# Kernel tuning notes

Measured on AMD Instinct MI355X. Metric: run time of the kernel, lower is better.

## Reference

```python
import jax, jax.numpy as jnp
import numpy as np

N = 100000
IN_C = 128
HID_C = 128
OUT_C = 128
E = 3200000


def setup_inputs() -> dict:
    key = jax.random.key(0)
    ks = jax.random.split(key, 8)
    x = jax.random.normal(ks[0], (N, IN_C), dtype=jnp.float32)
    edge_index = jax.random.randint(ks[1], (2, E), 0, N, dtype=jnp.int64)
    edge_weight = jnp.ones((E,), dtype=jnp.float32)
    s = 1.0 / np.sqrt(HID_C)
    W_conv = jax.random.uniform(ks[2], (HID_C, IN_C), jnp.float32, -s, s)
    b_conv = jnp.zeros((HID_C,), dtype=jnp.float32)
    W_fc = jax.random.uniform(ks[3], (HID_C, HID_C), jnp.float32, -s, s)
    b_fc = jax.random.uniform(ks[4], (HID_C,), jnp.float32, -s, s)
    W_fc2 = jax.random.uniform(ks[5], (OUT_C, HID_C), jnp.float32, -s, s)
    b_fc2 = jax.random.uniform(ks[6], (OUT_C,), jnp.float32, -s, s)
    return {"x": x, "edge_index": edge_index, "edge_weight": edge_weight,
            "W_conv": W_conv, "b_conv": b_conv, "W_fc": W_fc, "b_fc": b_fc,
            "W_fc2": W_fc2, "b_fc2": b_fc2}


def _gcn_conv(x, edge_index, edge_weight, W_conv, b_conv):
    n = x.shape[0]
    # add self-loops with weight 1 (PyG GCNConv default)
    loop = jnp.arange(n, dtype=edge_index.dtype)
    src = jnp.concatenate([edge_index[0], loop])
    dst = jnp.concatenate([edge_index[1], loop])
    ew = jnp.concatenate([edge_weight, jnp.ones((n,), dtype=edge_weight.dtype)])
    # symmetric normalization: deg^-1/2[src] * w * deg^-1/2[dst]
    deg = jax.ops.segment_sum(ew, dst, num_segments=n)
    dinv = jnp.where(deg > 0, jax.lax.rsqrt(jnp.where(deg > 0, deg, 1.0)), 0.0)
    norm = dinv[src] * ew * dinv[dst]  # [E+N]
    h = x @ W_conv.T                   # [N, hid], bias-free linear first
    msg = h[src] * norm[:, None]       # gather + scale
    agg = jax.ops.segment_sum(msg, dst, num_segments=n)  # scatter-add
    return agg + b_conv


def reference(x, edge_index, edge_weight, W_conv, b_conv, W_fc, b_fc, W_fc2, b_fc2):
    h = _gcn_conv(x, edge_index, edge_weight, W_conv, b_conv)
    h = jax.nn.relu(h)
    h = jax.nn.relu(h @ W_fc.T + b_fc)
    return h @ W_fc2.T + b_fc2
```

## Files before the change

kernel.cpp:

```cpp
#include <hip/hip_runtime.h>

typedef short bf16x8 __attribute__((ext_vector_type(8)));
typedef short bf16x4 __attribute__((ext_vector_type(4)));
typedef float f32x4 __attribute__((ext_vector_type(4)));
typedef float f32x2 __attribute__((ext_vector_type(2)));

#define PS 32
#define CAPP 1312
#define NB 256
#define CAPB 17536

__device__ __forceinline__ unsigned short f2bf(float f) {
    unsigned int u = __float_as_uint(f);
    u = (u + 0x7FFFu + ((u >> 16) & 1u)) >> 16;
    return (unsigned short)u;
}

__global__ __launch_bounds__(1024) void scatA_k(const int* __restrict__ ei,
                                                const float* __restrict__ ew,
                                                int* __restrict__ bucketCnt,
                                                int2* __restrict__ bstage,
                                                const float* __restrict__ Wc,
                                                const float* __restrict__ Wf,
                                                const float* __restrict__ W2,
                                                unsigned short* __restrict__ wcb,
                                                unsigned short* __restrict__ wfb,
                                                unsigned short* __restrict__ w2b,
                                                int E, int NBK, int EPB) {
    __shared__ int cntl[256];
    __shared__ int basel[256];
    const int b = blockIdx.x, tid = threadIdx.x;

    if (b < 12) {
        int t = (b << 10) | tid;
        int a = t >> 12, idx = t & 4095;
        const float4* s4 = (const float4*)(a == 0 ? Wc : (a == 1 ? Wf : W2));
        unsigned short* dw = (a == 0 ? wcb : (a == 1 ? wfb : w2b));
        float4 v = s4[idx];
        ushort4 o;
        o.x = f2bf(v.x); o.y = f2bf(v.y); o.z = f2bf(v.z); o.w = f2bf(v.w);
        *(ushort4*)(dw + idx * 4) = o;
    }

    if (tid < 256) cntl[tid] = 0;
    __syncthreads();
    const int s = b * EPB, e = min(E, s + EPB);
    for (int i = s + tid; i < e; i += 1024)
        atomicAdd(&cntl[ei[E + i] >> 9], 1);
    __syncthreads();
    if (tid < NBK) {
        int c = cntl[tid];
        basel[tid] = tid * CAPB + (c ? atomicAdd(&bucketCnt[tid], c) : 0);
        cntl[tid] = 0;
    }
    __syncthreads();
    for (int i = s + tid; i < e; i += 1024) {
        int src = ei[i];
        int dst = ei[E + i];
        float w = ew[i];
        int bk = dst >> 9;
        int lidx = atomicAdd(&cntl[bk], 1);
        int pos = basel[bk] + lidx;
        if (pos < (bk + 1) * CAPB)
            bstage[pos] = make_int2(src | ((dst & 511) << 17), __float_as_int(w));
    }
}

__global__ __launch_bounds__(1024) void scatB_k(const int* __restrict__ bucketCnt,
                                                const int2* __restrict__ bstage,
                                                int* __restrict__ partCnt,
                                                int* __restrict__ nodeOff,
                                                float* __restrict__ dinv,
                                                int2* __restrict__ regions,
                                                int P, int N) {
    __shared__ int cnode[512];
    __shared__ float degf[512];
    const int bk = blockIdx.x, tid = threadIdx.x;
    const int cnt = min(bucketCnt[bk], CAPB);
    const int2* bs = bstage + (size_t)bk * CAPB;

    if (tid < 512) { cnode[tid] = 0; degf[tid] = 0.f; }
    __syncthreads();
    for (int i = tid; i < cnt; i += 1024) {
        int2 r = bs[i];
        int nl = ((unsigned)r.x >> 17) & 511;
        atomicAdd(&cnode[nl], 1);
        atomicAdd(&degf[nl], __int_as_float(r.y));
    }
    __syncthreads();
    if (tid < 512) {
        int cn = cnode[tid];
        int v = cn;
#pragma unroll
        for (int off = 1; off < 32; off <<= 1) {
            int u = __shfl_up(v, off, 32);
            if ((tid & 31) >= off) v += u;
        }
        int n = bk * 512 + tid;
        if (n < N) {
            nodeOff[n] = v - cn;
            dinv[n] = rsqrtf(1.0f + degf[tid]);
        }
        if ((tid & 31) == 31) {
            int p = bk * 16 + (tid >> 5);
            if (p < P) partCnt[p] = v;
        }
        cnode[tid] = v - cn;
    }
    __syncthreads();
    for (int i = tid; i < cnt; i += 1024) {
        int2 r = bs[i];
        unsigned x = (unsigned)r.x;
        int nl = (x >> 17) & 511;
        int pos = atomicAdd(&cnode[nl], 1);
        if (pos < CAPP) {
            int p = bk * 16 + (nl >> 5);
            regions[(size_t)p * CAPP + pos] = make_int2((int)((x & 0x1FFFFu) << 7), r.y);
        }
    }
}

__global__ __launch_bounds__(256) void dgemm1_k(const float* __restrict__ x,
                                                const unsigned short* __restrict__ Wcb,
                                                const float* __restrict__ dinv,
                                                unsigned short* __restrict__ h,
                                                int M) {
    __shared__ __align__(16) unsigned short Wl[128 * 136];
    __shared__ float dl64[64];
    const int tid = threadIdx.x;

    if (tid < 64) {
        int node = blockIdx.x * 64 + tid;
        dl64[tid] = (node < M) ? dinv[node] : 0.f;
    }

#pragma unroll
    for (int i = 0; i < 8; ++i) {
        int c = i * 256 + tid;
        int r = c >> 4, col = (c & 15) * 8;
        *(bf16x8*)&Wl[r * 136 + col] = *(const bf16x8*)(Wcb + c * 8);
    }
    __syncthreads();

    const int wave = tid >> 6, lane = tid & 63;
    const int m = lane & 15, quad = lane >> 4;
    const int rowBase = blockIdx.x * 64 + wave * 16;
    int arow = rowBase + m;
    int arowc = arow < M ? arow : (M - 1);

    bf16x8 afrag[4];
    const float* pa = x + (size_t)arowc * 128 + quad * 8;
#pragma unroll
    for (int kc = 0; kc < 4; ++kc) {
        float4 v0 = *(const float4*)(pa + kc * 32);
        float4 v1 = *(const float4*)(pa + kc * 32 + 4);
        bf16x8 f;
        f[0] = (short)f2bf(v0.x); f[1] = (short)f2bf(v0.y);
        f[2] = (short)f2bf(v0.z); f[3] = (short)f2bf(v0.w);
        f[4] = (short)f2bf(v1.x); f[5] = (short)f2bf(v1.y);
        f[6] = (short)f2bf(v1.z); f[7] = (short)f2bf(v1.w);
        afrag[kc] = f;
    }

    float dv[4];
#pragma unroll
    for (int r = 0; r < 4; ++r)
        dv[r] = dl64[wave * 16 + quad * 4 + r];

#pragma unroll
    for (int nt = 0; nt < 8; ++nt) {
        f32x4 acc = {0.f, 0.f, 0.f, 0.f};
        const unsigned short* wb = &Wl[(nt * 16 + m) * 136 + quad * 8];
#pragma unroll
        for (int kc = 0; kc < 4; ++kc) {
            bf16x8 bfrag = *(const bf16x8*)(wb + kc * 32);
            acc = __builtin_amdgcn_mfma_f32_16x16x32_bf16(afrag[kc], bfrag, acc, 0, 0, 0);
        }
        const int col = nt * 16 + m;
#pragma unroll
        for (int r = 0; r < 4; ++r) {
            int row = rowBase + quad * 4 + r;
            if (row < M)
                h[((size_t)(col >> 6) * M + row) * 64 + (col & 63)] = f2bf(acc[r] * dv[r]);
        }
    }
}

__global__ __launch_bounds__(256) void aggF_k(const int* __restrict__ partCnt,
                                              const int* __restrict__ nodeOff,
                                              const int2* __restrict__ regions,
                                              const unsigned short* __restrict__ h,
                                              const float* __restrict__ dinv,
                                              const float* __restrict__ bconv,
                                              unsigned short* __restrict__ h2, int N) {
    __shared__ __align__(16) int2 stag[CAPP];
    __shared__ int cstart[PS + 1];
    const int p = blockIdx.x, tid = threadIdx.x;
    const int cnt = min(partCnt[p], CAPP);
    const int2* reg = regions + (size_t)p * CAPP;

    if (tid < PS) {
        int node = p * PS + tid;
        cstart[tid] = (node < N) ? nodeOff[node] : cnt;
    } else if (tid == PS) {
        cstart[PS] = cnt;
    }
    for (int i = tid; i < cnt; i += 256) stag[i] = reg[i];
    __syncthreads();

    const int wave = tid >> 6, lane = tid & 63;
    const int g = lane >> 4;
    const int c4 = (lane & 15) * 4;
    const int c4b = c4 * 2;

#define ACC2(q, w) {                                                        \
        unsigned ux = (unsigned)(q).x, uy = (unsigned)(q).y;                \
        f32x2 ww; ww[0] = (w); ww[1] = (w);                                 \
        f32x2 v01, v23;                                                     \
        v01[0] = __uint_as_float(ux << 16);                                 \
        v01[1] = __uint_as_float(ux & 0xFFFF0000u);                         \
        v23[0] = __uint_as_float(uy << 16);                                 \
        v23[1] = __uint_as_float(uy & 0xFFFF0000u);                         \
        a01 = v01 * ww + a01; a23 = v23 * ww + a23; }

#pragma unroll
    for (int hh = 0; hh < 2; ++hh) {
        const char* hb = (const char*)h + ((size_t)hh * (size_t)N << 7);
        for (int nl = wave; nl < PS; nl += 4) {
            int n = p * PS + nl;
            if (n >= N) continue;
            const int s = cstart[nl], e = cstart[nl + 1];
            f32x2 a01 = {0.f, 0.f}, a23 = {0.f, 0.f};
            int j = s;
            const int e32 = s + ((e - s) & ~31);
            for (; j < e32; j += 32) {
                int2 r0 = stag[j + g];
                int2 r1 = stag[j + 4 + g];
                int2 r2 = stag[j + 8 + g];
                int2 r3 = stag[j + 12 + g];
                int2 r4 = stag[j + 16 + g];
                int2 r5 = stag[j + 20 + g];
                int2 r6 = stag[j + 24 + g];
                int2 r7 = stag[j + 28 + g];
                int2 q0 = *(const int2*)(hb + ((unsigned)r0.x + c4b));
                int2 q1 = *(const int2*)(hb + ((unsigned)r1.x + c4b));
                int2 q2 = *(const int2*)(hb + ((unsigned)r2.x + c4b));
                int2 q3 = *(const int2*)(hb + ((unsigned)r3.x + c4b));
                int2 q4 = *(const int2*)(hb + ((unsigned)r4.x + c4b));
                int2 q5 = *(const int2*)(hb + ((unsigned)r5.x + c4b));
                int2 q6 = *(const int2*)(hb + ((unsigned)r6.x + c4b));
                int2 q7 = *(const int2*)(hb + ((unsigned)r7.x + c4b));
                ACC2(q0, __int_as_float(r0.y));
                ACC2(q1, __int_as_float(r1.y));
                ACC2(q2, __int_as_float(r2.y));
                ACC2(q3, __int_as_float(r3.y));
                ACC2(q4, __int_as_float(r4.y));
                ACC2(q5, __int_as_float(r5.y));
                ACC2(q6, __int_as_float(r6.y));
                ACC2(q7, __int_as_float(r7.y));
            }
            const int e16 = s + ((e - s) & ~15);
            for (; j < e16; j += 16) {
                int2 r0 = stag[j + g];
                int2 r1 = stag[j + 4 + g];
                int2 r2 = stag[j + 8 + g];
                int2 r3 = stag[j + 12 + g];
                int2 q0 = *(const int2*)(hb + ((unsigned)r0.x + c4b));
                int2 q1 = *(const int2*)(hb + ((unsigned)r1.x + c4b));
                int2 q2 = *(const int2*)(hb + ((unsigned)r2.x + c4b));
                int2 q3 = *(const int2*)(hb + ((unsigned)r3.x + c4b));
                ACC2(q0, __int_as_float(r0.y));
                ACC2(q1, __int_as_float(r1.y));
                ACC2(q2, __int_as_float(r2.y));
                ACC2(q3, __int_as_float(r3.y));
            }
            for (; j < e; j += 8) {
                int j0 = j + g, j1 = j + 4 + g;
                int2 r0 = stag[j0 < e ? j0 : s];
                int2 r1 = stag[j1 < e ? j1 : s];
                float w0 = (j0 < e) ? __int_as_float(r0.y) : 0.f;
                float w1 = (j1 < e) ? __int_as_float(r1.y) : 0.f;
                int2 q0 = *(const int2*)(hb + ((unsigned)r0.x + c4b));
                int2 q1 = *(const int2*)(hb + ((unsigned)r1.x + c4b));
                ACC2(q0, w0);
                ACC2(q1, w1);
            }
            float acc[4] = {a01[0], a01[1], a23[0], a23[1]};
#pragma unroll
            for (int k = 0; k < 4; ++k) {
                float v = acc[k];
                v += __shfl_xor(v, 16, 64);
                v += __shfl_xor(v, 32, 64);
                acc[k] = v;
            }
            if (g == 0) {
                float di = dinv[n];
                int2 qs = *(const int2*)(hb + (((size_t)(unsigned)n << 7) + c4b));
                float4 b = *(const float4*)(bconv + hh * 64 + c4);
                unsigned ux = (unsigned)qs.x, uy = (unsigned)qs.y;
                bf16x4 o;
                o[0] = (short)f2bf(fmaxf(di * (acc[0] + __uint_as_float(ux << 16)) + b.x, 0.f));
                o[1] = (short)f2bf(fmaxf(di * (acc[1] + __uint_as_float(ux & 0xFFFF0000u)) + b.y, 0.f));
                o[2] = (short)f2bf(fmaxf(di * (acc[2] + __uint_as_float(uy << 16)) + b.z, 0.f));
                o[3] = (short)f2bf(fmaxf(di * (acc[3] + __uint_as_float(uy & 0xFFFF0000u)) + b.w, 0.f));
                *(bf16x4*)(h2 + (size_t)n * 128 + hh * 64 + c4) = o;
            }
        }
    }
#undef ACC2
}

__global__ __launch_bounds__(256) void gemm23_k(const unsigned short* __restrict__ h2,
                                                const unsigned short* __restrict__ Wfb,
                                                const float* __restrict__ bfc,
                                                const unsigned short* __restrict__ W2b,
                                                const float* __restrict__ b2,
                                                float* __restrict__ out, int M) {
    __shared__ __align__(16) unsigned short Wl[128 * 136];
    __shared__ __align__(16) unsigned short Tl[64 * 136];
    const int tid = threadIdx.x;

#pragma unroll
    for (int i = 0; i < 8; ++i) {
        int c = i * 256 + tid;
        int r = c >> 4, col = (c & 15) * 8;
        *(bf16x8*)&Wl[r * 136 + col] = *(const bf16x8*)(Wfb + c * 8);
    }
    __syncthreads();

    const int wave = tid >> 6, lane = tid & 63;
    const int m = lane & 15, quad = lane >> 4;
    const int rowBase = blockIdx.x * 64 + wave * 16;
    int arow = rowBase + m;
    int arowc = arow < M ? arow : (M - 1);

    bf16x8 afrag[4];
    {
        const unsigned short* pa = h2 + (size_t)arowc * 128 + quad * 8;
#pragma unroll
        for (int kc = 0; kc < 4; ++kc)
            afrag[kc] = *(const bf16x8*)(pa + kc * 32);
    }

#pragma unroll
    for (int nt = 0; nt < 8; ++nt) {
        f32x4 acc = {0.f, 0.f, 0.f, 0.f};
        const unsigned short* wb = &Wl[(nt * 16 + m) * 136 + quad * 8];
#pragma unroll
        for (int kc = 0; kc < 4; ++kc) {
            bf16x8 bfrag = *(const bf16x8*)(wb + kc * 32);
            acc = __builtin_amdgcn_mfma_f32_16x16x32_bf16(afrag[kc], bfrag, acc, 0, 0, 0);
        }
        const int col = nt * 16 + m;
        float bv = bfc[col];
#pragma unroll
        for (int r = 0; r < 4; ++r) {
            int rowl = wave * 16 + quad * 4 + r;
            Tl[rowl * 136 + col] = f2bf(fmaxf(acc[r] + bv, 0.f));
        }
    }
    __syncthreads();

#pragma unroll
    for (int i = 0; i < 8; ++i) {
        int c = i * 256 + tid;
        int r = c >> 4, col = (c & 15) * 8;
        *(bf16x8*)&Wl[r * 136 + col] = *(const bf16x8*)(W2b + c * 8);
    }
    __syncthreads();

    bf16x8 afrag2[4];
    {
        const unsigned short* pa = &Tl[(wave * 16 + m) * 136 + quad * 8];
#pragma unroll
        for (int kc = 0; kc < 4; ++kc)
            afrag2[kc] = *(const bf16x8*)(pa + kc * 32);
    }
#pragma unroll
    for (int nt = 0; nt < 8; ++nt) {
        f32x4 acc = {0.f, 0.f, 0.f, 0.f};
        const unsigned short* wb = &Wl[(nt * 16 + m) * 136 + quad * 8];
#pragma unroll
        for (int kc = 0; kc < 4; ++kc) {
            bf16x8 bfrag = *(const bf16x8*)(wb + kc * 32);
            acc = __builtin_amdgcn_mfma_f32_16x16x32_bf16(afrag2[kc], bfrag, acc, 0, 0, 0);
        }
        const int col = nt * 16 + m;
        float bv = b2[col];
#pragma unroll
        for (int r = 0; r < 4; ++r) {
            int row = rowBase + quad * 4 + r;
            if (row < M)
                out[(size_t)row * 128 + col] = acc[r] + bv;
        }
    }
}

extern "C" void kernel_launch(void* const* d_in, const int* in_sizes, int n_in,
                              void* d_out, int out_size, void* d_ws, size_t ws_size,
                              hipStream_t stream) {
    const float* x  = (const float*)d_in[0];
    const int* ei   = (const int*)d_in[1];
    const float* ew = (const float*)d_in[2];
    const float* Wc = (const float*)d_in[3];
    const float* bc = (const float*)d_in[4];
    const float* Wf = (const float*)d_in[5];
    const float* bf = (const float*)d_in[6];
    const float* W2 = (const float*)d_in[7];
    const float* b2 = (const float*)d_in[8];
    float* out = (float*)d_out;

    const int N = in_sizes[0] / 128;
    const int E = in_sizes[2];
    const int P = (N + PS - 1) / PS;
    const int NBK = (N + 511) >> 9;

    auto align256 = [](size_t v) { return (v + 255) & ~(size_t)255; };
    char* ws = (char*)d_ws;
    size_t off = 0;
    float* dinv  = (float*)(ws + off); off += align256((size_t)N * 4);
    int* nodeOff = (int*)(ws + off);   off += align256((size_t)N * 4);
    int* partCnt = (int*)(ws + off);   off += align256((size_t)P * 4);
    int* bucketCnt = (int*)(ws + off); off += align256((size_t)NBK * 4);
    unsigned short* wcb = (unsigned short*)(ws + off); off += align256(16384 * 2);
    unsigned short* wfb = (unsigned short*)(ws + off); off += align256(16384 * 2);
    unsigned short* w2b = (unsigned short*)(ws + off); off += align256(16384 * 2);
    unsigned short* h  = (unsigned short*)(ws + off); off += (size_t)N * 256;
    unsigned short* h2 = (unsigned short*)(ws + off);

    int2* bstage = (int2*)h;

    int2* regions = (int2*)out;

    const int EPB = (E + NB - 1) / NB;

    hipMemsetAsync(bucketCnt, 0, (size_t)NBK * 4, stream);
    scatA_k<<<NB, 1024, 0, stream>>>(ei, ew, bucketCnt, bstage, Wc, Wf, W2, wcb, wfb, w2b, E, NBK, EPB);
    scatB_k<<<NBK, 1024, 0, stream>>>(bucketCnt, bstage, partCnt, nodeOff, dinv, regions, P, N);
    dgemm1_k<<<(N + 63) / 64, 256, 0, stream>>>(x, wcb, dinv, h, N);
    aggF_k<<<P, 256, 0, stream>>>(partCnt, nodeOff, regions, h, dinv, bc, h2, N);
    gemm23_k<<<(N + 63) / 64, 256, 0, stream>>>(h2, wfb, bf, w2b, b2, out, N);
}
```

Before: 353.1 us.

## Fuse first GEMM into scatter kernel and defer per-node sorting to aggregation

The first GEMM (x·Wc) is merged into the edge-bucketing kernel as extra blocks, so it runs concurrently with the scatter instead of as a separate launch after it. Because h no longer depends on dinv, the source-side normalization moves into aggF, which applies dinv[src] to each edge weight while staging, and the self-loop term is scaled by di². scatB now writes only per-partition cursors with the local node id packed into each entry, and aggF does the per-node ordering through shared-memory atomics. bstage is relocated to the h2 region so it no longer aliases h. The cost is an extra dinv gather per edge in aggF and a larger fused kernel whose blocks contend for resources.

```diff
diff --git a/kernel.cpp b/kernel.cpp
--- a/kernel.cpp
+++ b/kernel.cpp
@@ -16,53 +16,107 @@
     return (unsigned short)u;
 }
 
-__global__ __launch_bounds__(1024) void scatA_k(const int* __restrict__ ei,
-                                                const float* __restrict__ ew,
-                                                int* __restrict__ bucketCnt,
-                                                int2* __restrict__ bstage,
-                                                const float* __restrict__ Wc,
-                                                const float* __restrict__ Wf,
-                                                const float* __restrict__ W2,
-                                                unsigned short* __restrict__ wcb,
-                                                unsigned short* __restrict__ wfb,
-                                                unsigned short* __restrict__ w2b,
-                                                int E, int NBK, int EPB) {
-    __shared__ int cntl[256];
-    __shared__ int basel[256];
+__global__ __launch_bounds__(1024) void mega_k(const int* __restrict__ ei,
+                                               const float* __restrict__ ew,
+                                               int* __restrict__ bucketCnt,
+                                               int2* __restrict__ bstage,
+                                               const float* __restrict__ x,
+                                               const float* __restrict__ Wc,
+                                               const float* __restrict__ Wf,
+                                               const float* __restrict__ W2,
+                                               unsigned short* __restrict__ wfb,
+                                               unsigned short* __restrict__ w2b,
+                                               unsigned short* __restrict__ h,
+                                               int E, int M, int NBK, int EPB) {
+    __shared__ __align__(16) unsigned short Wl[128 * 136];
     const int b = blockIdx.x, tid = threadIdx.x;
 
-    if (b < 12) {
-        int t = (b << 10) | tid;
-        int a = t >> 12, idx = t & 4095;
-        const float4* s4 = (const float4*)(a == 0 ? Wc : (a == 1 ? Wf : W2));
-        unsigned short* dw = (a == 0 ? wcb : (a == 1 ? wfb : w2b));
-        float4 v = s4[idx];
-        ushort4 o;
-        o.x = f2bf(v.x); o.y = f2bf(v.y); o.z = f2bf(v.z); o.w = f2bf(v.w);
-        *(ushort4*)(dw + idx * 4) = o;
-    }
-
-    if (tid < 256) cntl[tid] = 0;
-    __syncthreads();
-    const int s = b * EPB, e = min(E, s + EPB);
-    for (int i = s + tid; i < e; i += 1024)
-        atomicAdd(&cntl[ei[E + i] >> 9], 1);
-    __syncthreads();
-    if (tid < NBK) {
-        int c = cntl[tid];
-        basel[tid] = tid * CAPB + (c ? atomicAdd(&bucketCnt[tid], c) : 0);
-        cntl[tid] = 0;
-    }
-    __syncthreads();
-    for (int i = s + tid; i < e; i += 1024) {
-        int src = ei[i];
-        int dst = ei[E + i];
-        float w = ew[i];
-        int bk = dst >> 9;
-        int lidx = atomicAdd(&cntl[bk], 1);
-        int pos = basel[bk] + lidx;
-        if (pos < (bk + 1) * CAPB)
-            bstage[pos] = make_int2(src | ((dst & 511) << 17), __float_as_int(w));
+    if (b < NB) {
+        int* cntl = (int*)Wl;
+        int* basel = cntl + 256;
+        if (b < 8) {
+            int t = (b << 10) | tid;
+            int a = t >> 12, idx = t & 4095;
+            const float4* s4 = (const float4*)(a == 0 ? Wf : W2);
+            unsigned short* dw = (a == 0 ? wfb : w2b);
+            float4 v = s4[idx];
+            ushort4 o;
+            o.x = f2bf(v.x); o.y = f2bf(v.y); o.z = f2bf(v.z); o.w = f2bf(v.w);
+            *(ushort4*)(dw + idx * 4) = o;
+        }
+        if (tid < 256) cntl[tid] = 0;
+        __syncthreads();
+        const int s = b * EPB, e = min(E, s + EPB);
+        for (int i = s + tid; i < e; i += 1024)
+            atomicAdd(&cntl[ei[E + i] >> 9], 1);
+        __syncthreads();
+        if (tid < NBK) {
+            int c = cntl[tid];
+            basel[tid] = tid * CAPB + (c ? atomicAdd(&bucketCnt[tid], c) : 0);
+            cntl[tid] = 0;
+        }
+        __syncthreads();
+        for (int i = s + tid; i < e; i += 1024) {
+            int src = ei[i];
+            int dst = ei[E + i];
+            float w = ew[i];
+            int bk = dst >> 9;
+            int lidx = atomicAdd(&cntl[bk], 1);
+            int pos = basel[bk] + lidx;
+            if (pos < (bk + 1) * CAPB)
+                bstage[pos] = make_int2(src | ((dst & 511) << 17), __float_as_int(w));
+        }
+    } else {
+        const int gb = b - NB;
+#pragma unroll
+        for (int i = 0; i < 4; ++i) {
+            int e4 = i * 1024 + tid;
+            float4 v = ((const float4*)Wc)[e4];
+            int el = e4 * 4, r = el >> 7, cc = el & 127;
+            unsigned short* pp = &Wl[r * 136 + cc];
+            pp[0] = f2bf(v.x); pp[1] = f2bf(v.y); pp[2] = f2bf(v.z); pp[3] = f2bf(v.w);
+        }
+        __syncthreads();
+
+        const int wave = tid >> 6, lane = tid & 63;
+        const int m = lane & 15, quad = lane >> 4;
+        const int rowBase = gb * 256 + wave * 16;
+        if (rowBase < M) {
+            int arow = rowBase + m;
+            int arowc = arow < M ? arow : (M - 1);
+
+            bf16x8 afrag[4];
+            const float* pa = x + (size_t)arowc * 128 + quad * 8;
+#pragma unroll
+            for (int kc = 0; kc < 4; ++kc) {
+                float4 v0 = *(const float4*)(pa + kc * 32);
+                float4 v1 = *(const float4*)(pa + kc * 32 + 4);
+                bf16x8 f;
+                f[0] = (short)f2bf(v0.x); f[1] = (short)f2bf(v0.y);
+                f[2] = (short)f2bf(v0.z); f[3] = (short)f2bf(v0.w);
+                f[4] = (short)f2bf(v1.x); f[5] = (short)f2bf(v1.y);
+                f[6] = (short)f2bf(v1.z); f[7] = (short)f2bf(v1.w);
+                afrag[kc] = f;
+            }
+
+#pragma unroll
+            for (int nt = 0; nt < 8; ++nt) {
+                f32x4 acc = {0.f, 0.f, 0.f, 0.f};
+                const unsigned short* wb = &Wl[(nt * 16 + m) * 136 + quad * 8];
+#pragma unroll
+                for (int kc = 0; kc < 4; ++kc) {
+                    bf16x8 bfrag = *(const bf16x8*)(wb + kc * 32);
+                    acc = __builtin_amdgcn_mfma_f32_16x16x32_bf16(afrag[kc], bfrag, acc, 0, 0, 0);
+                }
+                const int col = nt * 16 + m;
+#pragma unroll
+                for (int r = 0; r < 4; ++r) {
+                    int row = rowBase + quad * 4 + r;
+                    if (row < M)
+                        h[((size_t)(col >> 6) * M + row) * 64 + (col & 63)] = f2bf(acc[r]);
+                }
+            }
+        }
     }
 }
 
@@ -75,11 +129,13 @@
                                                 int P, int N) {
     __shared__ int cnode[512];
     __shared__ float degf[512];
+    __shared__ int cur[16];
     const int bk = blockIdx.x, tid = threadIdx.x;
     const int cnt = min(bucketCnt[bk], CAPB);
     const int2* bs = bstage + (size_t)bk * CAPB;
 
     if (tid < 512) { cnode[tid] = 0; degf[tid] = 0.f; }
+    if (tid < 16) cur[tid] = 0;
     __syncthreads();
     for (int i = tid; i < cnt; i += 1024) {
         int2 r = bs[i];
@@ -105,83 +161,18 @@
             int p = bk * 16 + (tid >> 5);
             if (p < P) partCnt[p] = v;
         }
-        cnode[tid] = v - cn;
     }
     __syncthreads();
     for (int i = tid; i < cnt; i += 1024) {
         int2 r = bs[i];
-        unsigned x = (unsigned)r.x;
-        int nl = (x >> 17) & 511;
-        int pos = atomicAdd(&cnode[nl], 1);
+        unsigned xx = (unsigned)r.x;
+        int nl = (xx >> 17) & 511;
+        int pl = nl >> 5;
+        int pos = atomicAdd(&cur[pl], 1);
         if (pos < CAPP) {
-            int p = bk * 16 + (nl >> 5);
-            regions[(size_t)p * CAPP + pos] = make_int2((int)((x & 0x1FFFFu) << 7), r.y);
-        }
-    }
-}
-
-__global__ __launch_bounds__(256) void dgemm1_k(const float* __restrict__ x,
-                                                const unsigned short* __restrict__ Wcb,
-                                                const float* __restrict__ dinv,
-                                                unsigned short* __restrict__ h,
-                                                int M) {
-    __shared__ __align__(16) unsigned short Wl[128 * 136];
-    __shared__ float dl64[64];
-    const int tid = threadIdx.x;
-
-    if (tid < 64) {
-        int node = blockIdx.x * 64 + tid;
-        dl64[tid] = (node < M) ? dinv[node] : 0.f;
-    }
-
-#pragma unroll
-    for (int i = 0; i < 8; ++i) {
-        int c = i * 256 + tid;
-        int r = c >> 4, col = (c & 15) * 8;
-        *(bf16x8*)&Wl[r * 136 + col] = *(const bf16x8*)(Wcb + c * 8);
-    }
-    __syncthreads();
-
-    const int wave = tid >> 6, lane = tid & 63;
-    const int m = lane & 15, quad = lane >> 4;
-    const int rowBase = blockIdx.x * 64 + wave * 16;
-    int arow = rowBase + m;
-    int arowc = arow < M ? arow : (M - 1);
-
-    bf16x8 afrag[4];
-    const float* pa = x + (size_t)arowc * 128 + quad * 8;
-#pragma unroll
-    for (int kc = 0; kc < 4; ++kc) {
-        float4 v0 = *(const float4*)(pa + kc * 32);
-        float4 v1 = *(const float4*)(pa + kc * 32 + 4);
-        bf16x8 f;
-        f[0] = (short)f2bf(v0.x); f[1] = (short)f2bf(v0.y);
-        f[2] = (short)f2bf(v0.z); f[3] = (short)f2bf(v0.w);
-        f[4] = (short)f2bf(v1.x); f[5] = (short)f2bf(v1.y);
-        f[6] = (short)f2bf(v1.z); f[7] = (short)f2bf(v1.w);
-        afrag[kc] = f;
-    }
-
-    float dv[4];
-#pragma unroll
-    for (int r = 0; r < 4; ++r)
-        dv[r] = dl64[wave * 16 + quad * 4 + r];
-
-#pragma unroll
-    for (int nt = 0; nt < 8; ++nt) {
-        f32x4 acc = {0.f, 0.f, 0.f, 0.f};
-        const unsigned short* wb = &Wl[(nt * 16 + m) * 136 + quad * 8];
-#pragma unroll
-        for (int kc = 0; kc < 4; ++kc) {
-            bf16x8 bfrag = *(const bf16x8*)(wb + kc * 32);
-            acc = __builtin_amdgcn_mfma_f32_16x16x32_bf16(afrag[kc], bfrag, acc, 0, 0, 0);
-        }
-        const int col = nt * 16 + m;
-#pragma unroll
-        for (int r = 0; r < 4; ++r) {
-            int row = rowBase + quad * 4 + r;
-            if (row < M)
-                h[((size_t)(col >> 6) * M + row) * 64 + (col & 63)] = f2bf(acc[r] * dv[r]);
+            int p = bk * 16 + pl;
+            regions[(size_t)p * CAPP + pos] =
+                make_int2((int)(xx & 0x1FFFFu) | ((nl & 31) << 24), r.y);
         }
     }
 }
@@ -195,17 +186,28 @@
                                               unsigned short* __restrict__ h2, int N) {
     __shared__ __align__(16) int2 stag[CAPP];
     __shared__ int cstart[PS + 1];
+    __shared__ int wcur[PS];
     const int p = blockIdx.x, tid = threadIdx.x;
     const int cnt = min(partCnt[p], CAPP);
     const int2* reg = regions + (size_t)p * CAPP;
 
     if (tid < PS) {
         int node = p * PS + tid;
-        cstart[tid] = (node < N) ? nodeOff[node] : cnt;
+        int o = (node < N) ? nodeOff[node] : cnt;
+        cstart[tid] = o;
+        wcur[tid] = o;
     } else if (tid == PS) {
         cstart[PS] = cnt;
     }
-    for (int i = tid; i < cnt; i += 256) stag[i] = reg[i];
+    __syncthreads();
+    for (int i = tid; i < cnt; i += 256) {
+        int2 r = reg[i];
+        unsigned xx = (unsigned)r.x;
+        int srcn = xx & 0xFFFFFF;
+        int pos = atomicAdd(&wcur[(xx >> 24) & 31], 1);
+        stag[pos] = make_int2(srcn << 7,
+                              __float_as_int(__int_as_float(r.y) * dinv[srcn]));
+    }
     __syncthreads();
 
     const int wave = tid >> 6, lane = tid & 63;
@@ -295,14 +297,15 @@
             }
             if (g == 0) {
                 float di = dinv[n];
+                float sc = di * di;
                 int2 qs = *(const int2*)(hb + (((size_t)(unsigned)n << 7) + c4b));
                 float4 b = *(const float4*)(bconv + hh * 64 + c4);
                 unsigned ux = (unsigned)qs.x, uy = (unsigned)qs.y;
                 bf16x4 o;
-                o[0] = (short)f2bf(fmaxf(di * (acc[0] + __uint_as_float(ux << 16)) + b.x, 0.f));
-                o[1] = (short)f2bf(fmaxf(di * (acc[1] + __uint_as_float(ux & 0xFFFF0000u)) + b.y, 0.f));
-                o[2] = (short)f2bf(fmaxf(di * (acc[2] + __uint_as_float(uy << 16)) + b.z, 0.f));
-                o[3] = (short)f2bf(fmaxf(di * (acc[3] + __uint_as_float(uy & 0xFFFF0000u)) + b.w, 0.f));
+                o[0] = (short)f2bf(fmaxf(di * acc[0] + sc * __uint_as_float(ux << 16) + b.x, 0.f));
+                o[1] = (short)f2bf(fmaxf(di * acc[1] + sc * __uint_as_float(ux & 0xFFFF0000u) + b.y, 0.f));
+                o[2] = (short)f2bf(fmaxf(di * acc[2] + sc * __uint_as_float(uy << 16) + b.z, 0.f));
+                o[3] = (short)f2bf(fmaxf(di * acc[3] + sc * __uint_as_float(uy & 0xFFFF0000u) + b.w, 0.f));
                 *(bf16x4*)(h2 + (size_t)n * 128 + hh * 64 + c4) = o;
             }
         }
@@ -422,22 +425,21 @@
     int* nodeOff = (int*)(ws + off);   off += align256((size_t)N * 4);
     int* partCnt = (int*)(ws + off);   off += align256((size_t)P * 4);
     int* bucketCnt = (int*)(ws + off); off += align256((size_t)NBK * 4);
-    unsigned short* wcb = (unsigned short*)(ws + off); off += align256(16384 * 2);
     unsigned short* wfb = (unsigned short*)(ws + off); off += align256(16384 * 2);
     unsigned short* w2b = (unsigned short*)(ws + off); off += align256(16384 * 2);
     unsigned short* h  = (unsigned short*)(ws + off); off += (size_t)N * 256;
     unsigned short* h2 = (unsigned short*)(ws + off);
-
-    int2* bstage = (int2*)h;
+    int2* bstage = (int2*)(ws + off);
 
     int2* regions = (int2*)out;
 
     const int EPB = (E + NB - 1) / NB;
+    const int GB = (N + 255) / 256;
 
     hipMemsetAsync(bucketCnt, 0, (size_t)NBK * 4, stream);
-    scatA_k<<<NB, 1024, 0, stream>>>(ei, ew, bucketCnt, bstage, Wc, Wf, W2, wcb, wfb, w2b, E, NBK, EPB);
+    mega_k<<<NB + GB, 1024, 0, stream>>>(ei, ew, bucketCnt, bstage, x, Wc, Wf, W2,
+                                         wfb, w2b, h, E, N, NBK, EPB);
     scatB_k<<<NBK, 1024, 0, stream>>>(bucketCnt, bstage, partCnt, nodeOff, dinv, regions, P, N);
-    dgemm1_k<<<(N + 63) / 64, 256, 0, stream>>>(x, wcb, dinv, h, N);
     aggF_k<<<P, 256, 0, stream>>>(partCnt, nodeOff, regions, h, dinv, bc, h2, N);
     gemm23_k<<<(N + 63) / 64, 256, 0, stream>>>(h2, wfb, bf, w2b, b2, out, N);
 }
```

Result: no change. 355.8 us (+0.8%).
